# Kernel tuning notes

Hardware: AMD Instinct MI355X
Metric: run time of the kernel (lower is better)

## Reference

```python
import jax, jax.numpy as jnp
import numpy as np

EPS = 1e-12  # torch F.normalize eps


def setup_inputs() -> dict:
    key = jax.random.key(0)
    ks = jax.random.split(key, 6)
    B, D, F, N, C, L = 4096, 1024, 1024, 8192, 64, 28
    features = jax.random.normal(ks[0], (B, D), dtype=jnp.float32)
    labels = (jax.random.uniform(ks[1], (B, L)) < 0.2).astype(jnp.float32)  # multi-label targets
    g_weight = jax.random.normal(ks[2], (F, D), dtype=jnp.float32) * 0.02  # nn.Linear weight [out,in]
    ex_features = jax.random.normal(ks[3], (N, D), dtype=jnp.float32)
    ex_class_reps = jax.random.uniform(ks[4], (N, C), dtype=jnp.float32) * 2.0 - 1.0
    class_reps = jax.random.uniform(ks[5], (L, C), dtype=jnp.float32) * 2.0 - 1.0
    return {"features": features, "labels": labels, "g_weight": g_weight,
            "ex_features": ex_features, "ex_class_reps": ex_class_reps,
            "class_reps": class_reps, "p_factor": 3}


def _l2norm(x):
    # torch F.normalize(dim=1): x / max(||x||_2, eps)
    n = jnp.sqrt(jnp.sum(x * x, axis=1, keepdims=True))
    return x / jnp.maximum(n, EPS)


def reference(features, labels, g_weight, ex_features, ex_class_reps, class_reps, p_factor):
    # g projection (bias=False)
    f = features @ g_weight.T            # [B, F]
    exf = ex_features @ g_weight.T       # [N, F]
    # cosine similarity: normalized matmul
    s = _l2norm(f) @ _l2norm(exf).T      # [B, N]
    # power-sign activation
    a = jnp.sign(s) * jnp.abs(s) ** p_factor
    # L1 normalize along exemplar axis
    a = a / jnp.maximum(jnp.sum(jnp.abs(a), axis=1, keepdims=True), EPS)
    # exemplar readout
    echo = a @ ex_class_reps             # [B, C]
    # cdist (euclidean) to class representatives -> negative distances as logits
    diff = echo[:, None, :] - class_reps[None, :, :]   # [B, L, C]
    neg_dists = -jnp.sqrt(jnp.sum(diff * diff, axis=-1))  # [B, L]
    # BCEWithLogitsLoss (mean reduction)
    x, y = neg_dists, labels
    loss = jnp.mean(jnp.maximum(x, 0.0) - x * y + jnp.log1p(jnp.exp(-jnp.abs(x))))
    return (loss, neg_dists)
```

## Files before the change

### kernel.cpp

```cpp
#include <hip/hip_runtime.h>
#include <math.h>

#define EPSN 1e-12f

typedef __attribute__((ext_vector_type(8))) short short8;
typedef __attribute__((ext_vector_type(4))) float f32x4;

__device__ __forceinline__ void split_hi_lo(float x, unsigned short& h, unsigned short& l)
{
    unsigned int xb = __float_as_uint(x);
    h = (unsigned short)(xb >> 16);
    float r = x - __uint_as_float(xb & 0xffff0000u);
    l = (unsigned short)(__float_as_uint(r) >> 16);
}

__device__ __forceinline__ unsigned short f2bf_rne(float x)
{
    unsigned int u = __float_as_uint(x);
    unsigned int r = u + 0x7fffu + ((u >> 16) & 1u);
    return (unsigned short)(r >> 16);
}

__device__ __forceinline__ void gload16(const void* g, void* l)
{
    __builtin_amdgcn_global_load_lds(
        (const __attribute__((address_space(1))) void*)g,
        (__attribute__((address_space(3))) void*)l, 16, 0, 0);
}

__device__ __forceinline__ short8 read_frag(const unsigned char* plane, int row, int chunk)
{
    int byte = row * 128 + ((chunk ^ (row & 7)) << 4);
    return *reinterpret_cast<const short8*>(plane + byte);
}

__device__ __forceinline__ void stage_split(const float* __restrict__ src, int K, int k0,
                                            unsigned char* hi_plane, unsigned char* lo_plane,
                                            int tid)
{
#pragma unroll
    for (int q = 0; q < 8; ++q) {
        int idx = tid + q * 256;
        int row = idx >> 4;
        int f4  = idx & 15;
        float4 v = *reinterpret_cast<const float4*>(&src[(size_t)row * K + k0 + f4 * 4]);
        unsigned short h[4], l[4];
        split_hi_lo(v.x, h[0], l[0]);
        split_hi_lo(v.y, h[1], l[1]);
        split_hi_lo(v.z, h[2], l[2]);
        split_hi_lo(v.w, h[3], l[3]);
        int byte = row * 128 + (((f4 >> 1) ^ (row & 7)) << 4) + (f4 & 1) * 8;
        *reinterpret_cast<ushort4*>(hi_plane + byte) = make_ushort4(h[0], h[1], h[2], h[3]);
        *reinterpret_cast<ushort4*>(lo_plane + byte) = make_ushort4(l[0], l[1], l[2], l[3]);
    }
}

__global__ __launch_bounds__(256)
void split_rows(const float* __restrict__ src, unsigned short* __restrict__ dst)
{
    const int row = blockIdx.x, tid = threadIdx.x;
    float4 v = reinterpret_cast<const float4*>(src + (size_t)row * 1024)[tid];
    unsigned short h[4], l[4];
    split_hi_lo(v.x, h[0], l[0]); split_hi_lo(v.y, h[1], l[1]);
    split_hi_lo(v.z, h[2], l[2]); split_hi_lo(v.w, h[3], l[3]);
    unsigned short* R = dst + (size_t)row * 2048;
    *reinterpret_cast<ushort4*>(R + tid * 4)        = make_ushort4(h[0], h[1], h[2], h[3]);
    *reinterpret_cast<ushort4*>(R + 1024 + tid * 4) = make_ushort4(l[0], l[1], l[2], l[3]);
}

__global__ __launch_bounds__(256)
void l2norm_split(float* __restrict__ X)
{
    const int row = blockIdx.x, tid = threadIdx.x;
    float* Xr = X + (size_t)row * 1024;
    float4 v = reinterpret_cast<float4*>(Xr)[tid];
    float s = v.x * v.x + v.y * v.y + v.z * v.z + v.w * v.w;
#pragma unroll
    for (int off = 32; off > 0; off >>= 1) s += __shfl_down(s, off);
    __shared__ float red[4];
    __shared__ float scale_sh;
    if ((tid & 63) == 0) red[tid >> 6] = s;
    __syncthreads();
    if (tid == 0) {
        float n = sqrtf(red[0] + red[1] + red[2] + red[3]);
        scale_sh = 1.f / fmaxf(n, EPSN);
    }
    __syncthreads();
    const float sc = scale_sh;
    v.x *= sc; v.y *= sc; v.z *= sc; v.w *= sc;
    unsigned short h[4], l[4];
    split_hi_lo(v.x, h[0], l[0]); split_hi_lo(v.y, h[1], l[1]);
    split_hi_lo(v.z, h[2], l[2]); split_hi_lo(v.w, h[3], l[3]);
    unsigned short* R = reinterpret_cast<unsigned short*>(Xr);
    *reinterpret_cast<ushort4*>(R + tid * 4)        = make_ushort4(h[0], h[1], h[2], h[3]);
    *reinterpret_cast<ushort4*>(R + 1024 + tid * 4) = make_ushort4(l[0], l[1], l[2], l[3]);
}

__global__ __launch_bounds__(256)
void transpose_exR(const float* __restrict__ exR, unsigned short* __restrict__ exT, int N)
{
    __shared__ unsigned short sm[64][256];
    const int tid = threadIdx.x;
    const int n0 = blockIdx.x * 256;
    const float4* src = reinterpret_cast<const float4*>(exR + (size_t)(n0 + tid) * 64);
#pragma unroll
    for (int q = 0; q < 16; ++q) {
        float4 v = src[q];
        sm[q * 4 + 0][tid] = f2bf_rne(v.x);
        sm[q * 4 + 1][tid] = f2bf_rne(v.y);
        sm[q * 4 + 2][tid] = f2bf_rne(v.z);
        sm[q * 4 + 3][tid] = f2bf_rne(v.w);
    }
    __syncthreads();
#pragma unroll
    for (int j = 0; j < 32; ++j) {
        int idx = tid + j * 256;
        int c = idx >> 7, nl2 = idx & 127;
        *reinterpret_cast<ushort2*>(exT + (size_t)c * N + n0 + nl2 * 2) =
            *reinterpret_cast<const ushort2*>(&sm[c][nl2 * 2]);
    }
}

__global__ __launch_bounds__(256, 2)
void gemm_w(const float* __restrict__ A, const unsigned short* __restrict__ spW,
            float* __restrict__ C, int Nn, int K)
{
    __shared__ __align__(16) unsigned char smem[65536];
    unsigned char* sA_hi = smem;
    unsigned char* sA_lo = smem + 16384;
    unsigned char* sB_hi = smem + 32768;
    unsigned char* sB_lo = smem + 49152;

    const int tid  = threadIdx.x;
    const int lane = tid & 63;
    const int wave = tid >> 6;
    const int wr = wave >> 1, wc = wave & 1;
    const int brow = blockIdx.y * 128;
    const int bcol = blockIdx.x * 128;
    const float* Abase = A + (size_t)brow * K;
    const char*  Wbase = (const char*)spW + (size_t)bcol * 4096;

    int offW[4];
#pragma unroll
    for (int i = 0; i < 4; ++i) {
        int t = (wave * 4 + i) * 64 + lane;
        int r = t >> 3, c = (t & 7) ^ (r & 7);
        offW[i] = r * 4096 + c * 16;
    }

    f32x4 acc[4][4] = {};

    for (int k0 = 0; k0 < K; k0 += 64) {
        const int k2 = k0 * 2;
#pragma unroll
        for (int i = 0; i < 4; ++i) {
            gload16(Wbase + offW[i] + k2,        sB_hi + (wave * 4 + i) * 1024);
            gload16(Wbase + offW[i] + 2048 + k2, sB_lo + (wave * 4 + i) * 1024);
        }
        stage_split(Abase, K, k0, sA_hi, sA_lo, tid);
        __syncthreads();
#pragma unroll
        for (int kk = 0; kk < 2; ++kk) {
            const int ch = kk * 4 + (lane >> 4);
            short8 bh[4], bl[4];
#pragma unroll
            for (int fn = 0; fn < 4; ++fn) {
                int rb = wc * 64 + fn * 16 + (lane & 15);
                bh[fn] = read_frag(sB_hi, rb, ch);
                bl[fn] = read_frag(sB_lo, rb, ch);
            }
#pragma unroll
            for (int fm = 0; fm < 4; ++fm) {
                int ra = wr * 64 + fm * 16 + (lane & 15);
                short8 ah = read_frag(sA_hi, ra, ch);
                short8 al = read_frag(sA_lo, ra, ch);
#pragma unroll
                for (int fn = 0; fn < 4; ++fn) {
                    acc[fm][fn] = __builtin_amdgcn_mfma_f32_16x16x32_bf16(ah, bh[fn], acc[fm][fn], 0, 0, 0);
                    acc[fm][fn] = __builtin_amdgcn_mfma_f32_16x16x32_bf16(ah, bl[fn], acc[fm][fn], 0, 0, 0);
                    acc[fm][fn] = __builtin_amdgcn_mfma_f32_16x16x32_bf16(al, bh[fn], acc[fm][fn], 0, 0, 0);
                }
            }
        }
        __syncthreads();
    }

#pragma unroll
    for (int fm = 0; fm < 4; ++fm)
#pragma unroll
        for (int fn = 0; fn < 4; ++fn)
#pragma unroll
            for (int reg = 0; reg < 4; ++reg) {
                int row = brow + wr * 64 + fm * 16 + (lane >> 4) * 4 + reg;
                int col = bcol + wc * 64 + fn * 16 + (lane & 15);
                C[(size_t)row * Nn + col] = acc[fm][fn][reg];
            }
}

__global__ __launch_bounds__(256, 2)
void fused_mfma2(const unsigned short* __restrict__ spnF,
                 const unsigned short* __restrict__ spnE,
                 const unsigned short* __restrict__ exT,
                 float* __restrict__ echo,
                 float* __restrict__ rowsum,
                 const int* __restrict__ p_ptr,
                 int N, int K)
{
    __shared__ __align__(16) unsigned char smem[65536];
    unsigned char* sA_hi = smem;
    unsigned char* sA_lo = smem + 16384;
    unsigned char* sB_hi = smem + 32768;
    unsigned char* sB_lo = smem + 49152;
    unsigned char* aS = smem;
    unsigned char* eT = smem + 49152;

    const int tid  = threadIdx.x;
    const int lane = tid & 63;
    const int wave = tid >> 6;
    const int wr = wave >> 1, wc = wave & 1;
    const int brow  = blockIdx.x * 128;
    const int ncol0 = blockIdx.y * 4 * 128;
    const int p = p_ptr[0];
    const char* Af  = (const char*)spnF + (size_t)brow * 4096;
    const char* eTb = (const char*)exT;

    int offA[4], offE[4];
#pragma unroll
    for (int i = 0; i < 4; ++i) {
        int t = (wave * 4 + i) * 64 + lane;
        int r = t >> 3, c = (t & 7) ^ (r & 7);
        offA[i] = r * 4096 + c * 16;
        int cc = t >> 4, chp = t & 15, c2 = chp ^ (cc & 7);
        offE[i] = cc * (2 * N) + c2 * 16;
    }

    f32x4 acc_e[2][4] = {};
    float rsum[4][4] = {};

    for (int nt = 0; nt < 4; ++nt) {
        const int ncol = ncol0 + nt * 128;
        const char* Bn = (const char*)spnE + (size_t)ncol * 4096;

        f32x4 acc[4][4] = {};
        for (int k0 = 0; k0 < K; k0 += 64) {
            const int k2 = k0 * 2;
#pragma unroll
            for (int i = 0; i < 4; ++i) {
                gload16(Af + offA[i] + k2,        sA_hi + (wave * 4 + i) * 1024);
                gload16(Af + offA[i] + 2048 + k2, sA_lo + (wave * 4 + i) * 1024);
                gload16(Bn + offA[i] + k2,        sB_hi + (wave * 4 + i) * 1024);
                gload16(Bn + offA[i] + 2048 + k2, sB_lo + (wave * 4 + i) * 1024);
            }
            __syncthreads();
#pragma unroll
            for (int kk = 0; kk < 2; ++kk) {
                const int ch = kk * 4 + (lane >> 4);
                short8 bh[4], bl[4];
#pragma unroll
                for (int fn2 = 0; fn2 < 4; ++fn2) {
                    int rb = wc * 64 + fn2 * 16 + (lane & 15);
                    bh[fn2] = read_frag(sB_hi, rb, ch);
                    bl[fn2] = read_frag(sB_lo, rb, ch);
                }
#pragma unroll
                for (int fm = 0; fm < 4; ++fm) {
                    int ra = wr * 64 + fm * 16 + (lane & 15);
                    short8 ah = read_frag(sA_hi, ra, ch);
                    short8 al = read_frag(sA_lo, ra, ch);
#pragma unroll
                    for (int fn2 = 0; fn2 < 4; ++fn2) {
                        acc[fm][fn2] = __builtin_amdgcn_mfma_f32_16x16x32_bf16(ah, bh[fn2], acc[fm][fn2], 0, 0, 0);
                        acc[fm][fn2] = __builtin_amdgcn_mfma_f32_16x16x32_bf16(ah, bl[fn2], acc[fm][fn2], 0, 0, 0);
                        acc[fm][fn2] = __builtin_amdgcn_mfma_f32_16x16x32_bf16(al, bh[fn2], acc[fm][fn2], 0, 0, 0);
                    }
                }
            }
            __syncthreads();
        }

#pragma unroll
        for (int i = 0; i < 4; ++i)
            gload16(eTb + offE[i] + ncol * 2, eT + (wave * 4 + i) * 1024);

#pragma unroll
        for (int fm = 0; fm < 4; ++fm)
#pragma unroll
            for (int reg = 0; reg < 4; ++reg) {
                int row = wr * 64 + fm * 16 + (lane >> 4) * 4 + reg;
#pragma unroll
                for (int fn2 = 0; fn2 < 4; ++fn2) {
                    int col = wc * 64 + fn2 * 16 + (lane & 15);
                    float s = acc[fm][fn2][reg];
                    float a;
                    if (p == 3) a = s * s * s;
                    else        a = copysignf(powf(fabsf(s), (float)p), s);
                    rsum[fm][reg] += fabsf(a);
                    int byte = row * 256 + (((col >> 3) ^ (row & 7)) << 4) + (col & 7) * 2;
                    *reinterpret_cast<unsigned short*>(aS + byte) = f2bf_rne(a);
                }
            }
        __syncthreads();

#pragma unroll
        for (int ks = 0; ks < 4; ++ks) {
            const int ch = ks * 4 + (lane >> 4);
            short8 bfr[4];
#pragma unroll
            for (int fn2 = 0; fn2 < 4; ++fn2) {
                int rc = fn2 * 16 + (lane & 15);
                int byte = rc * 256 + ((ch ^ (rc & 7)) << 4);
                bfr[fn2] = *reinterpret_cast<const short8*>(eT + byte);
            }
#pragma unroll
            for (int fm2 = 0; fm2 < 2; ++fm2) {
                int ra = wave * 32 + fm2 * 16 + (lane & 15);
                int byte = ra * 256 + ((ch ^ (ra & 7)) << 4);
                short8 af = *reinterpret_cast<const short8*>(aS + byte);
#pragma unroll
                for (int fn2 = 0; fn2 < 4; ++fn2)
                    acc_e[fm2][fn2] = __builtin_amdgcn_mfma_f32_16x16x32_bf16(af, bfr[fn2], acc_e[fm2][fn2], 0, 0, 0);
            }
        }
        __syncthreads();
    }

#pragma unroll
    for (int fm2 = 0; fm2 < 2; ++fm2)
#pragma unroll
        for (int fn2 = 0; fn2 < 4; ++fn2)
#pragma unroll
            for (int reg = 0; reg < 4; ++reg) {
                int row = brow + wave * 32 + fm2 * 16 + (lane >> 4) * 4 + reg;
                int col = fn2 * 16 + (lane & 15);
                atomicAdd(&echo[(size_t)row * 64 + col], acc_e[fm2][fn2][reg]);
            }

#pragma unroll
    for (int fm = 0; fm < 4; ++fm)
#pragma unroll
        for (int reg = 0; reg < 4; ++reg) {
            float v = rsum[fm][reg];
            v += __shfl_xor(v, 1);
            v += __shfl_xor(v, 2);
            v += __shfl_xor(v, 4);
            v += __shfl_xor(v, 8);
            if ((lane & 15) == 0) {
                int row = brow + wr * 64 + fm * 16 + (lane >> 4) * 4 + reg;
                atomicAdd(&rowsum[row], v);
            }
        }
}

__global__ __launch_bounds__(256)
void finalize_kernel(const float* __restrict__ echo, const float* __restrict__ rowsum,
                     const float* __restrict__ class_reps,
                     const float* __restrict__ labels,
                     float* __restrict__ out,
                     float* __restrict__ loss_acc,
                     int B, int L, int C)
{
    extern __shared__ float cr[];
    const int tid = threadIdx.x;
    for (int i = tid; i < L * C; i += 256) cr[i] = class_reps[i];
    __syncthreads();

    const int row = blockIdx.x * 256 + tid;
    float lsum = 0.f;
    if (row < B) {
        const float inv = 1.f / fmaxf(rowsum[row], EPSN);
        float e[64];
        const float4* er = reinterpret_cast<const float4*>(echo + (size_t)row * 64);
#pragma unroll
        for (int q = 0; q < 16; ++q) {
            float4 v = er[q];
            e[q * 4 + 0] = v.x * inv; e[q * 4 + 1] = v.y * inv;
            e[q * 4 + 2] = v.z * inv; e[q * 4 + 3] = v.w * inv;
        }
        for (int l = 0; l < L; ++l) {
            float d = 0.f;
#pragma unroll
            for (int c = 0; c < 64; ++c) {
                float t = e[c] - cr[l * 64 + c];
                d += t * t;
            }
            float x = -sqrtf(d);
            out[1 + (size_t)row * L + l] = x;
            float y = labels[(size_t)row * L + l];
            lsum += fmaxf(x, 0.f) - x * y + log1pf(expf(-fabsf(x)));
        }
    }
#pragma unroll
    for (int off = 32; off > 0; off >>= 1) lsum += __shfl_down(lsum, off);
    __shared__ float red[4];
    if ((tid & 63) == 0) red[tid >> 6] = lsum;
    __syncthreads();
    if (tid == 0) atomicAdd(loss_acc, red[0] + red[1] + red[2] + red[3]);
}

__global__ void write_loss(const float* __restrict__ loss_acc,
                           float* __restrict__ out, float invBL)
{
    out[0] = loss_acc[0] * invBL;
}

extern "C" void kernel_launch(void* const* d_in, const int* in_sizes, int n_in,
                              void* d_out, int out_size, void* d_ws, size_t ws_size,
                              hipStream_t stream)
{
    const float* features    = (const float*)d_in[0];
    const float* labels      = (const float*)d_in[1];
    const float* g_weight    = (const float*)d_in[2];
    const float* ex_features = (const float*)d_in[3];
    const float* ex_reps     = (const float*)d_in[4];
    const float* class_reps  = (const float*)d_in[5];
    const int*   p_ptr       = (const int*)d_in[6];

    const int D = 1024;
    const int B = in_sizes[0] / D;
    const int F = in_sizes[2] / D;
    const int N = in_sizes[3] / D;
    const int C = in_sizes[4] / N;
    const int L = in_sizes[5] / C;

    char* ws = (char*)d_ws;
    float*          Xf     = (float*)(ws);
    float*          Xe     = (float*)(ws + (size_t)B * 4096);
    unsigned short* sp_w   = (unsigned short*)(ws + (size_t)(B + N) * 4096);
    unsigned short* exT    = (unsigned short*)(ws + (size_t)(B + N + F) * 4096);
    float*          echo   = (float*)(ws + (size_t)(B + N + F) * 4096 + (size_t)64 * N * 2);
    float*          rsums  = echo + (size_t)B * C;
    float*          loss_a = rsums + B;

    hipMemsetAsync(echo, 0, (size_t)(B * C + B + 4) * 4, stream);

    split_rows<<<F, 256, 0, stream>>>(g_weight, sp_w);
    transpose_exR<<<N / 256, 256, 0, stream>>>(ex_reps, exT, N);

    {
        dim3 g1(F / 128, B / 128);
        gemm_w<<<g1, 256, 0, stream>>>(features, sp_w, Xf, F, D);
        dim3 g2(F / 128, N / 128);
        gemm_w<<<g2, 256, 0, stream>>>(ex_features, sp_w, Xe, F, D);
    }
    l2norm_split<<<B, 256, 0, stream>>>(Xf);
    l2norm_split<<<N, 256, 0, stream>>>(Xe);

    {
        dim3 g(B / 128, 16);
        fused_mfma2<<<g, 256, 0, stream>>>((const unsigned short*)Xf,
                                           (const unsigned short*)Xe,
                                           exT, echo, rsums, p_ptr, N, F);
    }

    {
        dim3 g((B + 255) / 256);
        size_t shb = (size_t)L * C * sizeof(float);
        finalize_kernel<<<g, 256, shb, stream>>>(echo, rsums, class_reps, labels,
                                                 (float*)d_out, loss_a, B, L, C);
    }
    write_loss<<<1, 1, 0, stream>>>(loss_a, (float*)d_out, 1.f / (float)(B * L));
}
```

Baseline: 445.6 us.

## Widen fused similarity tile to 128x256 with K=32 steps and direct-global readout

The fused cosine-similarity/readout kernel now computes 128x256 output tiles per pass (two passes per block instead of four 128x128 passes), stepping K by 32 with a new swizzle for smaller LDS stage buffers. Each wave holds a 4x8 accumulator grid, so every B fragment is reused across four A fragments. The exemplar class-rep operand for the readout GEMM is read straight from global memory instead of being staged in LDS. Row-sum and echo atomics are issued per pass rather than once at the end. The larger accumulator set raises register pressure and may reduce occupancy, while K=32 steps double the number of barriers per tile.

New measurement: 1.598 ms. 259% more time.

```diff
diff --git a/kernel.cpp b/kernel.cpp
--- a/kernel.cpp
+++ b/kernel.cpp
@@ -55,6 +55,12 @@
     }
 }
 
+__device__ __forceinline__ short8 read_frag32(const unsigned char* plane, int row, int ch)
+{
+    int byte = row * 64 + ((ch ^ ((row >> 1) & 3)) << 4);
+    return *reinterpret_cast<const short8*>(plane + byte);
+}
+
 __global__ __launch_bounds__(256)
 void split_rows(const float* __restrict__ src, unsigned short* __restrict__ dst)
 {
@@ -198,7 +204,7 @@
 }
 
 __global__ __launch_bounds__(256, 2)
-void fused_mfma2(const unsigned short* __restrict__ spnF,
+void fused_mfma5(const unsigned short* __restrict__ spnF,
                  const unsigned short* __restrict__ spnE,
                  const unsigned short* __restrict__ exT,
                  float* __restrict__ echo,
@@ -206,149 +212,137 @@
                  const int* __restrict__ p_ptr,
                  int N, int K)
 {
-    __shared__ __align__(16) unsigned char smem[65536];
-    unsigned char* sA_hi = smem;
-    unsigned char* sA_lo = smem + 16384;
-    unsigned char* sB_hi = smem + 32768;
-    unsigned char* sB_lo = smem + 49152;
-    unsigned char* aS = smem;
-    unsigned char* eT = smem + 49152;
+    __shared__ __align__(16) unsigned char S[65536];
+    unsigned char* sA_hi = S;
+    unsigned char* sA_lo = S + 8192;
+    unsigned char* sB_hi = S + 16384;
+    unsigned char* sB_lo = S + 32768;
+    unsigned char* aS    = S;
 
     const int tid  = threadIdx.x;
     const int lane = tid & 63;
     const int wave = tid >> 6;
     const int wr = wave >> 1, wc = wave & 1;
+    const int l15 = lane & 15, lh = lane >> 4;
     const int brow  = blockIdx.x * 128;
-    const int ncol0 = blockIdx.y * 4 * 128;
+    const int ncol0 = blockIdx.y * 512;
     const int p = p_ptr[0];
-    const char* Af  = (const char*)spnF + (size_t)brow * 4096;
-    const char* eTb = (const char*)exT;
-
-    int offA[4], offE[4];
-#pragma unroll
-    for (int i = 0; i < 4; ++i) {
-        int t = (wave * 4 + i) * 64 + lane;
-        int r = t >> 3, c = (t & 7) ^ (r & 7);
-        offA[i] = r * 4096 + c * 16;
-        int cc = t >> 4, chp = t & 15, c2 = chp ^ (cc & 7);
-        offE[i] = cc * (2 * N) + c2 * 16;
-    }
-
-    f32x4 acc_e[2][4] = {};
-    float rsum[4][4] = {};
-
-    for (int nt = 0; nt < 4; ++nt) {
-        const int ncol = ncol0 + nt * 128;
+    const char* Af = (const char*)spnF + (size_t)brow * 4096;
+
+    int srcA[2], srcB[4];
+#pragma unroll
+    for (int q = 0; q < 2; ++q) {
+        int t = tid + q * 256; int row = t >> 2;
+        srcA[q] = row * 4096 + ((t & 3) ^ ((row >> 1) & 3)) * 16;
+    }
+#pragma unroll
+    for (int q = 0; q < 4; ++q) {
+        int t = tid + q * 256; int row = t >> 2;
+        srcB[q] = row * 4096 + ((t & 3) ^ ((row >> 1) & 3)) * 16;
+    }
+
+    const int nk = K / 32;
+
+    for (int nt = 0; nt < 2; ++nt) {
+        const int ncol = ncol0 + nt * 256;
         const char* Bn = (const char*)spnE + (size_t)ncol * 4096;
 
-        f32x4 acc[4][4] = {};
-        for (int k0 = 0; k0 < K; k0 += 64) {
-            const int k2 = k0 * 2;
-#pragma unroll
-            for (int i = 0; i < 4; ++i) {
-                gload16(Af + offA[i] + k2,        sA_hi + (wave * 4 + i) * 1024);
-                gload16(Af + offA[i] + 2048 + k2, sA_lo + (wave * 4 + i) * 1024);
-                gload16(Bn + offA[i] + k2,        sB_hi + (wave * 4 + i) * 1024);
-                gload16(Bn + offA[i] + 2048 + k2, sB_lo + (wave * 4 + i) * 1024);
+        f32x4 acc[4][8] = {};
+        for (int k = 0; k < nk; ++k) {
+            const int kb = k * 64;
+#pragma unroll
+            for (int q = 0; q < 2; ++q) {
+                gload16(Af + srcA[q] + kb,        sA_hi + wave * 1024 + q * 4096);
+                gload16(Af + srcA[q] + 2048 + kb, sA_lo + wave * 1024 + q * 4096);
+            }
+#pragma unroll
+            for (int q = 0; q < 4; ++q) {
+                gload16(Bn + srcB[q] + kb,        sB_hi + wave * 1024 + q * 4096);
+                gload16(Bn + srcB[q] + 2048 + kb, sB_lo + wave * 1024 + q * 4096);
             }
             __syncthreads();
-#pragma unroll
-            for (int kk = 0; kk < 2; ++kk) {
-                const int ch = kk * 4 + (lane >> 4);
-                short8 bh[4], bl[4];
-#pragma unroll
-                for (int fn2 = 0; fn2 < 4; ++fn2) {
-                    int rb = wc * 64 + fn2 * 16 + (lane & 15);
-                    bh[fn2] = read_frag(sB_hi, rb, ch);
-                    bl[fn2] = read_frag(sB_lo, rb, ch);
+
+            short8 ah[4], al[4];
+#pragma unroll
+            for (int fm = 0; fm < 4; ++fm) {
+                int ra = wr * 64 + fm * 16 + l15;
+                ah[fm] = read_frag32(sA_hi, ra, lh);
+                al[fm] = read_frag32(sA_lo, ra, lh);
+            }
+#pragma unroll
+            for (int fn = 0; fn < 8; ++fn) {
+                int rb = wc * 128 + fn * 16 + l15;
+                short8 bh = read_frag32(sB_hi, rb, lh);
+                short8 bl = read_frag32(sB_lo, rb, lh);
+#pragma unroll
+                for (int fm = 0; fm < 4; ++fm) {
+                    acc[fm][fn] = __builtin_amdgcn_mfma_f32_16x16x32_bf16(ah[fm], bh, acc[fm][fn], 0, 0, 0);
+                    acc[fm][fn] = __builtin_amdgcn_mfma_f32_16x16x32_bf16(ah[fm], bl, acc[fm][fn], 0, 0, 0);
+                    acc[fm][fn] = __builtin_amdgcn_mfma_f32_16x16x32_bf16(al[fm], bh, acc[fm][fn], 0, 0, 0);
                 }
-#pragma unroll
-                for (int fm = 0; fm < 4; ++fm) {
-                    int ra = wr * 64 + fm * 16 + (lane & 15);
-                    short8 ah = read_frag(sA_hi, ra, ch);
-                    short8 al = read_frag(sA_lo, ra, ch);
-#pragma unroll
-                    for (int fn2 = 0; fn2 < 4; ++fn2) {
-                        acc[fm][fn2] = __builtin_amdgcn_mfma_f32_16x16x32_bf16(ah, bh[fn2], acc[fm][fn2], 0, 0, 0);
-                        acc[fm][fn2] = __builtin_amdgcn_mfma_f32_16x16x32_bf16(ah, bl[fn2], acc[fm][fn2], 0, 0, 0);
-                        acc[fm][fn2] = __builtin_amdgcn_mfma_f32_16x16x32_bf16(al, bh[fn2], acc[fm][fn2], 0, 0, 0);
-                    }
-                }
             }
             __syncthreads();
         }
 
 #pragma unroll
-        for (int i = 0; i < 4; ++i)
-            gload16(eTb + offE[i] + ncol * 2, eT + (wave * 4 + i) * 1024);
-
-#pragma unroll
         for (int fm = 0; fm < 4; ++fm)
 #pragma unroll
             for (int reg = 0; reg < 4; ++reg) {
-                int row = wr * 64 + fm * 16 + (lane >> 4) * 4 + reg;
-#pragma unroll
-                for (int fn2 = 0; fn2 < 4; ++fn2) {
-                    int col = wc * 64 + fn2 * 16 + (lane & 15);
-                    float s = acc[fm][fn2][reg];
+                int row = wr * 64 + fm * 16 + lh * 4 + reg;
+                float rs = 0.f;
+#pragma unroll
+                for (int fn = 0; fn < 8; ++fn) {
+                    int col = wc * 128 + fn * 16 + l15;
+                    float s = acc[fm][fn][reg];
                     float a;
                     if (p == 3) a = s * s * s;
                     else        a = copysignf(powf(fabsf(s), (float)p), s);
-                    rsum[fm][reg] += fabsf(a);
-                    int byte = row * 256 + (((col >> 3) ^ (row & 7)) << 4) + (col & 7) * 2;
+                    rs += fabsf(a);
+                    int byte = row * 512 + (((col >> 3) ^ (row & 7)) << 4) + (col & 7) * 2;
                     *reinterpret_cast<unsigned short*>(aS + byte) = f2bf_rne(a);
                 }
+                rs += __shfl_xor(rs, 1);
+                rs += __shfl_xor(rs, 2);
+                rs += __shfl_xor(rs, 4);
+                rs += __shfl_xor(rs, 8);
+                if (l15 == 0) atomicAdd(&rowsum[brow + row], rs);
             }
         __syncthreads();
 
-#pragma unroll
-        for (int ks = 0; ks < 4; ++ks) {
-            const int ch = ks * 4 + (lane >> 4);
+        f32x4 acc_e[2][4] = {};
+#pragma unroll
+        for (int ks = 0; ks < 8; ++ks) {
+            int kn = ncol + ks * 32 + lh * 8;
             short8 bfr[4];
 #pragma unroll
             for (int fn2 = 0; fn2 < 4; ++fn2) {
-                int rc = fn2 * 16 + (lane & 15);
-                int byte = rc * 256 + ((ch ^ (rc & 7)) << 4);
-                bfr[fn2] = *reinterpret_cast<const short8*>(eT + byte);
+                int c = fn2 * 16 + l15;
+                bfr[fn2] = *reinterpret_cast<const short8*>(exT + (size_t)c * N + kn);
             }
 #pragma unroll
             for (int fm2 = 0; fm2 < 2; ++fm2) {
-                int ra = wave * 32 + fm2 * 16 + (lane & 15);
-                int byte = ra * 256 + ((ch ^ (ra & 7)) << 4);
+                int ra = wave * 32 + fm2 * 16 + l15;
+                int ch2 = ks * 4 + lh;
+                int byte = ra * 512 + ((ch2 ^ (ra & 7)) << 4);
                 short8 af = *reinterpret_cast<const short8*>(aS + byte);
 #pragma unroll
                 for (int fn2 = 0; fn2 < 4; ++fn2)
                     acc_e[fm2][fn2] = __builtin_amdgcn_mfma_f32_16x16x32_bf16(af, bfr[fn2], acc_e[fm2][fn2], 0, 0, 0);
             }
         }
+
+#pragma unroll
+        for (int fm2 = 0; fm2 < 2; ++fm2)
+#pragma unroll
+            for (int fn2 = 0; fn2 < 4; ++fn2)
+#pragma unroll
+                for (int reg = 0; reg < 4; ++reg) {
+                    int row = brow + wave * 32 + fm2 * 16 + lh * 4 + reg;
+                    int col = fn2 * 16 + l15;
+                    atomicAdd(&echo[(size_t)row * 64 + col], acc_e[fm2][fn2][reg]);
+                }
         __syncthreads();
     }
-
-#pragma unroll
-    for (int fm2 = 0; fm2 < 2; ++fm2)
-#pragma unroll
-        for (int fn2 = 0; fn2 < 4; ++fn2)
-#pragma unroll
-            for (int reg = 0; reg < 4; ++reg) {
-                int row = brow + wave * 32 + fm2 * 16 + (lane >> 4) * 4 + reg;
-                int col = fn2 * 16 + (lane & 15);
-                atomicAdd(&echo[(size_t)row * 64 + col], acc_e[fm2][fn2][reg]);
-            }
-
-#pragma unroll
-    for (int fm = 0; fm < 4; ++fm)
-#pragma unroll
-        for (int reg = 0; reg < 4; ++reg) {
-            float v = rsum[fm][reg];
-            v += __shfl_xor(v, 1);
-            v += __shfl_xor(v, 2);
-            v += __shfl_xor(v, 4);
-            v += __shfl_xor(v, 8);
-            if ((lane & 15) == 0) {
-                int row = brow + wr * 64 + fm * 16 + (lane >> 4) * 4 + reg;
-                atomicAdd(&rowsum[row], v);
-            }
-        }
 }
 
 __global__ __launch_bounds__(256)
@@ -442,12 +436,13 @@
         dim3 g2(F / 128, N / 128);
         gemm_w<<<g2, 256, 0, stream>>>(ex_features, sp_w, Xe, F, D);
     }
+
     l2norm_split<<<B, 256, 0, stream>>>(Xf);
     l2norm_split<<<N, 256, 0, stream>>>(Xe);
 
     {
-        dim3 g(B / 128, 16);
-        fused_mfma2<<<g, 256, 0, stream>>>((const unsigned short*)Xf,
+        dim3 g(B / 128, N / 512);
+        fused_mfma5<<<g, 256, 0, stream>>>((const unsigned short*)Xf,
                                            (const unsigned short*)Xe,
                                            exT, echo, rsums, p_ptr, N, F);
     }
```
